# Performance work log

Measured on AMD Instinct MI355X. Metric: run time of the kernel, lower is better.

The kernel has to match this reference:

```python
import jax, jax.numpy as jnp
import numpy as np

B, S, H = 2, 2048, 2048
NH, NKV = 16, 4
HD = H // NH            # 128
GROUPS = NH // NKV      # 4
ROTARY_BASE = 10000.0
NEG = -1e9


def setup_inputs() -> dict:
    key = jax.random.key(0)
    ks = jax.random.split(key, 6)
    x = jax.random.normal(ks[0], (B, S, H), dtype=jnp.float32)
    # additive causal mask [B,1,S,S]
    causal = jnp.where(jnp.tril(jnp.ones((S, S), dtype=bool)), 0.0, NEG).astype(jnp.float32)
    attention_mask = jnp.broadcast_to(causal[None, None], (B, 1, S, S))
    position_ids = jnp.broadcast_to(jnp.arange(S, dtype=jnp.int32)[None], (B, S))
    sc = 0.02
    Wq = jax.random.normal(ks[1], (H, NH * HD), dtype=jnp.float32) * sc
    Wk = jax.random.normal(ks[2], (H, NKV * HD), dtype=jnp.float32) * sc
    Wv = jax.random.normal(ks[3], (H, NKV * HD), dtype=jnp.float32) * sc
    Wo = jax.random.normal(ks[4], (H, H), dtype=jnp.float32) * sc
    return {"x": x, "attention_mask": attention_mask, "position_ids": position_ids,
            "Wq": Wq, "Wk": Wk, "Wv": Wv, "Wo": Wo}


def _rotate_half(t):
    t1, t2 = t[..., : HD // 2], t[..., HD // 2:]
    return jnp.concatenate((-t2, t1), axis=-1)


def _rope_sin_cos(position_ids, dtype):
    inv_freq = 1.0 / (ROTARY_BASE ** (jnp.arange(0, HD, 2, dtype=jnp.float32) / HD))  # [HD/2]
    freqs = position_ids.astype(jnp.float32)[..., None] * inv_freq[None, None, :]      # [B,S,HD/2]
    emb = jnp.concatenate((freqs, freqs), axis=-1)                                     # [B,S,HD]
    return jnp.sin(emb).astype(dtype), jnp.cos(emb).astype(dtype)


def reference(x, attention_mask, position_ids, Wq, Wk, Wv, Wo):
    # QKV projections (no bias)
    q = (x @ Wq).reshape(B, S, NH, HD).transpose(0, 2, 1, 3)     # [B,NH,S,HD]
    k = (x @ Wk).reshape(B, S, NKV, HD).transpose(0, 2, 1, 3)    # [B,NKV,S,HD]
    v = (x @ Wv).reshape(B, S, NKV, HD).transpose(0, 2, 1, 3)
    sin, cos = _rope_sin_cos(position_ids, x.dtype)
    sin, cos = sin[:, None], cos[:, None]                         # unsqueeze head dim
    q = q * cos + _rotate_half(q) * sin
    k = k * cos + _rotate_half(k) * sin
    # GQA: repeat kv heads
    k = jnp.repeat(k, GROUPS, axis=1)                             # [B,NH,S,HD]
    v = jnp.repeat(v, GROUPS, axis=1)
    scores = jnp.einsum('bhqd,bhkd->bhqk', q, k) / jnp.sqrt(jnp.asarray(HD, x.dtype))
    scores = scores + attention_mask                              # additive causal mask
    attn = jax.nn.softmax(scores.astype(jnp.float32), axis=-1).astype(x.dtype)
    # dropout p=0.0 -> no-op
    out = jnp.einsum('bhqk,bhkd->bhqd', attn, v)                  # [B,NH,S,HD]
    out = out.transpose(0, 2, 1, 3).reshape(B, S, H)
    return out @ Wo
```

## Files before the change

kernel.cpp:

```cpp
#include <hip/hip_runtime.h>
#include <hip/hip_bf16.h>
#include <stdint.h>
#include <math.h>

#define B_ 2
#define S_ 2048
#define H_ 2048
#define NH_ 16
#define NKV_ 4
#define HD_ 128

typedef __bf16 bf16;
typedef __bf16 bf16x8 __attribute__((ext_vector_type(8)));
typedef __bf16 bf16x4 __attribute__((ext_vector_type(4)));
typedef float f32x4 __attribute__((ext_vector_type(4)));

__device__ __forceinline__ void async_copy16(const void* g, void* l) {
  __builtin_amdgcn_global_load_lds(
      (const __attribute__((address_space(1))) void*)(uintptr_t)g,
      (__attribute__((address_space(3))) void*)(uintptr_t)l,
      16, 0, 0);
}

__device__ __forceinline__ f32x4 mfma16(bf16x8 a, bf16x8 b, f32x4 c) {
  return __builtin_amdgcn_mfma_f32_16x16x32_bf16(a, b, c, 0, 0, 0);
}


__global__ void f32_to_bf16_k(const float* __restrict__ in, bf16* __restrict__ o, int n) {
  int i = (blockIdx.x * 256 + threadIdx.x) * 4;
  if (i >= n) return;
  float4 v = *(const float4*)(in + i);
  bf16x4 r;
  r[0] = (bf16)v.x; r[1] = (bf16)v.y; r[2] = (bf16)v.z; r[3] = (bf16)v.w;
  *(bf16x4*)(o + i) = r;
}

__global__ void transpose_to_bf16_k(const float* __restrict__ W, bf16* __restrict__ Wt,
                                    int K, int N) {
  __shared__ float tile[32][33];
  int n0 = blockIdx.x * 32, k0 = blockIdx.y * 32;
  int tx = threadIdx.x, ty = threadIdx.y;
#pragma unroll
  for (int j = 0; j < 32; j += 8)
    tile[ty + j][tx] = W[(size_t)(k0 + ty + j) * N + n0 + tx];
  __syncthreads();
#pragma unroll
  for (int j = 0; j < 32; j += 8)
    Wt[(size_t)(n0 + ty + j) * K + k0 + tx] = (bf16)tile[tx][ty + j];
}

__global__ void rope_table_k(float2* __restrict__ tab) {
  int i = blockIdx.x * 256 + threadIdx.x;
  int p = i >> 6, d = i & 63;
  float invf = expf(-((float)(2 * d) / 128.0f) * 9.210340371976184f);
  float fr = (float)p * invf;
  float sv, cv;
  sincosf(fr, &sv, &cv);
  tab[i] = make_float2(cv, sv);
}

__global__ void rope_apply_k(bf16* __restrict__ t, const int* __restrict__ pos_ids,
                             const float2* __restrict__ tab, int hshift, int hmask,
                             float scale) {
  int i = blockIdx.x * 256 + threadIdx.x;
  int d = i & 63;
  int tmp = i >> 6;
  int h = tmp & hmask;
  int row = tmp >> hshift;
  int pos = pos_ids[row];
  float2 cs = tab[pos * 64 + d];
  size_t base = (((size_t)row << hshift) + h) * HD_;
  float a = (float)t[base + d];
  float b = (float)t[base + d + 64];
  t[base + d]      = (bf16)((a * cs.x - b * cs.y) * scale);
  t[base + d + 64] = (bf16)((b * cs.x + a * cs.y) * scale);
}


template <int MODE>
__global__ __launch_bounds__(512) void gemm8_k(const bf16* __restrict__ A,
                                               const bf16* __restrict__ Bt,
                                               void* __restrict__ C0,
                                               void* __restrict__ C1,
                                               void* __restrict__ C2,
                                               int M, int N, int K) {
  extern __shared__ __align__(16) char smem[];
  const int tid = threadIdx.x;
  const int lane = tid & 63;
  const int w = tid >> 6;
  const int wm = w >> 2;
  const int wn = w & 3;
  const int g16 = lane >> 4, c16 = lane & 15;
  const int row0 = blockIdx.y * 128;
  const int col0 = blockIdx.x * 256;
  const int srow = tid >> 3;
  const int sslot = tid & 7;
  const int ldsw = w * 1024;

  auto stageA = [&](int s, int kt, int r) {
    int row = r * 64 + srow;
    int ss = sslot ^ (row & 7);
    async_copy16(A + (size_t)(row0 + row) * K + (kt << 6) + ss * 8,
                 smem + s * 49152 + r * 8192 + ldsw);
  };
  auto stageB = [&](int s, int kt, int r) {
    int row = r * 64 + srow;
    int ss = sslot ^ (row & 7);
    async_copy16(Bt + (size_t)(col0 + row) * K + (kt << 6) + ss * 8,
                 smem + s * 49152 + 16384 + r * 8192 + ldsw);
  };

  int offA[2][4], offB[2][4];
#pragma unroll
  for (int ks = 0; ks < 2; ++ks) {
#pragma unroll
    for (int i = 0; i < 4; ++i) {
      int ra = wm * 64 + i * 16 + c16;
      offA[ks][i] = ra * 128 + (((ks * 4 + g16) ^ (ra & 7)) << 4);
      int rb = wn * 64 + i * 16 + c16;
      offB[ks][i] = rb * 128 + (((ks * 4 + g16) ^ (rb & 7)) << 4);
    }
  }

  const f32x4 fz = {0.f, 0.f, 0.f, 0.f};
  f32x4 acc[4][4];
#pragma unroll
  for (int i = 0; i < 4; ++i)
#pragma unroll
    for (int j = 0; j < 4; ++j) acc[i][j] = fz;

  const int nkt = K >> 6;
#pragma unroll
  for (int r = 0; r < 2; ++r) stageA(0, 0, r);
#pragma unroll
  for (int r = 0; r < 4; ++r) stageB(0, 0, r);
#pragma unroll
  for (int r = 0; r < 2; ++r) stageA(1, 1, r);
#pragma unroll
  for (int r = 0; r < 4; ++r) stageB(1, 1, r);
  asm volatile("s_waitcnt vmcnt(6)" ::: "memory");
  __builtin_amdgcn_s_barrier();

  int ct = 0, pt = 2;
  for (int t = 0; t < nkt; ++t) {
    const char* Ab = smem + ct * 49152;
    const char* Bb = Ab + 16384;
    const bool pf = (t + 2 < nkt);
    const int kpf = t + 2;
    bf16x8 af[4], bfr[4];

#pragma unroll
    for (int i = 0; i < 4; ++i) af[i] = *(const bf16x8*)(Ab + offA[0][i]);
#pragma unroll
    for (int j = 0; j < 4; ++j) bfr[j] = *(const bf16x8*)(Bb + offB[0][j]);
    if (pf) { stageA(pt, kpf, 0); stageA(pt, kpf, 1); stageB(pt, kpf, 0); }
    __builtin_amdgcn_s_barrier();
    asm volatile("s_waitcnt lgkmcnt(0)" ::: "memory");
    __builtin_amdgcn_sched_barrier(0);
    __builtin_amdgcn_s_setprio(1);
#pragma unroll
    for (int i = 0; i < 4; ++i)
#pragma unroll
      for (int j = 0; j < 4; ++j) acc[i][j] = mfma16(af[i], bfr[j], acc[i][j]);
    __builtin_amdgcn_s_setprio(0);
    __builtin_amdgcn_sched_barrier(0);
    __builtin_amdgcn_s_barrier();

#pragma unroll
    for (int i = 0; i < 4; ++i) af[i] = *(const bf16x8*)(Ab + offA[1][i]);
#pragma unroll
    for (int j = 0; j < 4; ++j) bfr[j] = *(const bf16x8*)(Bb + offB[1][j]);
    if (pf) { stageB(pt, kpf, 1); stageB(pt, kpf, 2); stageB(pt, kpf, 3); }
    if (pf) asm volatile("s_waitcnt vmcnt(6)" ::: "memory");
    else    asm volatile("s_waitcnt vmcnt(0)" ::: "memory");
    __builtin_amdgcn_s_barrier();
    asm volatile("s_waitcnt lgkmcnt(0)" ::: "memory");
    __builtin_amdgcn_sched_barrier(0);
    __builtin_amdgcn_s_setprio(1);
#pragma unroll
    for (int i = 0; i < 4; ++i)
#pragma unroll
      for (int j = 0; j < 4; ++j) acc[i][j] = mfma16(af[i], bfr[j], acc[i][j]);
    __builtin_amdgcn_s_setprio(0);
    __builtin_amdgcn_sched_barrier(0);
    __builtin_amdgcn_s_barrier();

    ct = (ct == 2) ? 0 : ct + 1;
    pt = (pt == 2) ? 0 : pt + 1;
  }

#pragma unroll
  for (int i = 0; i < 4; ++i) {
    int gr0 = row0 + wm * 64 + i * 16 + g16 * 4;
#pragma unroll
    for (int j = 0; j < 4; ++j) {
      int gc = col0 + wn * 64 + j * 16 + c16;
      if constexpr (MODE == 2) {
        if (col0 < 2048) {
#pragma unroll
          for (int r = 0; r < 4; ++r)
            ((bf16*)C0)[(size_t)(gr0 + r) * 2048 + gc] = (bf16)acc[i][j][r];
        } else if (col0 < 2560) {
#pragma unroll
          for (int r = 0; r < 4; ++r)
            ((bf16*)C1)[(size_t)(gr0 + r) * 512 + (gc - 2048)] = (bf16)acc[i][j][r];
        } else {
          int dv = gc - 2560;
          int hkv = dv >> 7, d = dv & 127;
          size_t va = (((size_t)(gr0 >> 11) * NKV_ + hkv) * HD_ + d) * S_ + (gr0 & 2047);
          bf16x4 pk;
#pragma unroll
          for (int r = 0; r < 4; ++r) pk[r] = (bf16)acc[i][j][r];
          *(bf16x4*)((bf16*)C2 + va) = pk;
        }
      } else {
#pragma unroll
        for (int r = 0; r < 4; ++r) {
          if constexpr (MODE == 1)
            ((float*)C0)[(size_t)(gr0 + r) * N + gc] = acc[i][j][r];
          else
            ((bf16*)C0)[(size_t)(gr0 + r) * N + gc] = (bf16)acc[i][j][r];
        }
      }
    }
  }
}


template <bool OUT_F32, bool VT_Z1>
__global__ __launch_bounds__(256) void gemm_bt_k(const bf16* __restrict__ A,
                                                 const bf16* __restrict__ Bt0,
                                                 const bf16* __restrict__ Bt1,
                                                 void* __restrict__ C0, void* __restrict__ C1,
                                                 int M, int N, int K) {
  const bf16* __restrict__ Bt = (blockIdx.z == 0) ? Bt0 : Bt1;
  void* C = (blockIdx.z == 0) ? C0 : C1;
  __shared__ __align__(16) bf16 As[128 * 64];
  __shared__ __align__(16) bf16 Bs[128 * 64];
  const int tid = threadIdx.x;
  const int lane = tid & 63;
  const int w = tid >> 6;
  const int wm = w >> 1, wn = w & 1;
  const int g16 = lane >> 4, c16 = lane & 15;
  const int row0 = blockIdx.y * 128;
  const int col0 = blockIdx.x * 128;
  const int sr = lane >> 3;
  const int st = lane & 7;
  const int ss = st ^ sr;

  const f32x4 fz = {0.f, 0.f, 0.f, 0.f};
  f32x4 acc[4][4];
#pragma unroll
  for (int i = 0; i < 4; ++i)
#pragma unroll
    for (int j = 0; j < 4; ++j) acc[i][j] = fz;

  const int nkt = K >> 6;
  for (int kt = 0; kt < nkt; ++kt) {
    const int k0 = kt << 6;
    __syncthreads();
#pragma unroll
    for (int c = 0; c < 4; ++c) {
      int rbase = w * 32 + c * 8;
      async_copy16(A + (size_t)(row0 + rbase + sr) * K + k0 + ss * 8,
                   (char*)As + rbase * 128);
      async_copy16(Bt + (size_t)(col0 + rbase + sr) * K + k0 + ss * 8,
                   (char*)Bs + rbase * 128);
    }
    __syncthreads();
#pragma unroll
    for (int ks = 0; ks < 2; ++ks) {
      bf16x8 af[4], bfr[4];
#pragma unroll
      for (int t = 0; t < 4; ++t) {
        int ra = wm * 64 + t * 16 + c16;
        af[t] = *(const bf16x8*)((const char*)As + ra * 128 + (((ks * 4 + g16) ^ (ra & 7)) << 4));
        int rb = wn * 64 + t * 16 + c16;
        bfr[t] = *(const bf16x8*)((const char*)Bs + rb * 128 + (((ks * 4 + g16) ^ (rb & 7)) << 4));
      }
#pragma unroll
      for (int i = 0; i < 4; ++i)
#pragma unroll
        for (int j = 0; j < 4; ++j) acc[i][j] = mfma16(af[i], bfr[j], acc[i][j]);
    }
  }

  const bool vt = VT_Z1 && (blockIdx.z == 1);
#pragma unroll
  for (int i = 0; i < 4; ++i) {
    int gr0 = row0 + wm * 64 + i * 16 + g16 * 4;
#pragma unroll
    for (int j = 0; j < 4; ++j) {
      int gc = col0 + wn * 64 + j * 16 + c16;
      if (vt) {
        size_t va = ((size_t)((gr0 >> 11) * NKV_ + (gc >> 7)) * HD_ + (gc & 127)) * S_ + (gr0 & 2047);
        bf16x4 pk;
#pragma unroll
        for (int r = 0; r < 4; ++r) pk[r] = (bf16)acc[i][j][r];
        *(bf16x4*)((bf16*)C + va) = pk;
      } else {
#pragma unroll
        for (int r = 0; r < 4; ++r) {
          if constexpr (OUT_F32)
            ((float*)C)[(size_t)(gr0 + r) * N + gc] = acc[i][j][r];
          else
            ((bf16*)C)[(size_t)(gr0 + r) * N + gc] = (bf16)acc[i][j][r];
        }
      }
    }
  }
}


__global__ __launch_bounds__(256, 2) void attn_fwd_k(const bf16* __restrict__ Qg,
                                                     const bf16* __restrict__ Kg,
                                                     const bf16* __restrict__ VTg,
                                                     bf16* __restrict__ Og) {
  __shared__ __align__(16) bf16 Ks[2][64 * 128];
  __shared__ __align__(16) bf16 Vt[2][128 * 64];

  const int tid = threadIdx.x;
  const int lane = tid & 63;
  const int w = tid >> 6;
  const int g16 = lane >> 4;
  const int c16 = lane & 15;

  int bid = blockIdx.x;
  int rr_ = bid >> 5, bh = bid & 31;
  int qb = (rr_ < 8) ? (15 - rr_) : (rr_ - 8);
  const int b = bh >> 4;
  const int h = bh & 15;
  const int hkv = h >> 2;
  const int q0 = qb * 128;
  const int qw = q0 + w * 32;

  bf16x8 qf[2][4];
#pragma unroll
  for (int nq = 0; nq < 2; ++nq)
#pragma unroll
    for (int ksq = 0; ksq < 4; ++ksq)
      qf[nq][ksq] = *(const bf16x8*)(Qg + ((size_t)(b * S_ + qw + nq * 16 + c16) * NH_ + h) * HD_ + (ksq * 4 + g16) * 8);

  float m_run[2] = {-1e30f, -1e30f};
  float l_run[2] = {0.f, 0.f};
  const f32x4 fz = {0.f, 0.f, 0.f, 0.f};
  f32x4 acc[2][8];
#pragma unroll
  for (int nq = 0; nq < 2; ++nq)
#pragma unroll
    for (int dt = 0; dt < 8; ++dt) acc[nq][dt] = fz;

  const size_t kbase = ((size_t)b * S_ * NKV_ + hkv) * HD_;
  const size_t vbase = ((size_t)(b * NKV_ + hkv)) * HD_ * S_;

  auto stage = [&](int buf, int kv0) {
#pragma unroll
    for (int rd = 0; rd < 4; ++rd) {
      int Lb = rd * 256 + w * 64;
      int row = (Lb + lane) >> 4;
      int ssl = (lane & 15) ^ (row & 7);
      async_copy16(Kg + kbase + (size_t)(kv0 + row) * (NKV_ * HD_) + ssl * 8,
                   (char*)&Ks[buf][0] + Lb * 16);
    }
#pragma unroll
    for (int rd = 0; rd < 4; ++rd) {
      int Lb = rd * 256 + w * 64;
      int row = (Lb + lane) >> 3;
      int ssl = (lane & 7) ^ (row & 7);
      async_copy16(VTg + vbase + (size_t)row * S_ + kv0 + ssl * 8,
                   (char*)&Vt[buf][0] + Lb * 16);
    }
  };

  const int ntiles = 2 * qb + 2;
  stage(0, 0);
  int cur = 0;

  for (int t = 0; t < ntiles; ++t) {
    __syncthreads();
    if (t + 1 < ntiles) stage(cur ^ 1, (t + 1) * 64);
    const int kv0 = t * 64;

    if (kv0 <= qw + 31) {
      const bf16* KsC = &Ks[cur][0];
      const bf16* VtC = &Vt[cur][0];

      f32x4 sc[2][4];
#pragma unroll
      for (int nq = 0; nq < 2; ++nq)
#pragma unroll
        for (int mt = 0; mt < 4; ++mt) sc[nq][mt] = fz;

      __builtin_amdgcn_s_setprio(1);
#pragma unroll
      for (int ksq = 0; ksq < 4; ++ksq) {
        bf16x8 kf[4];
#pragma unroll
        for (int mt = 0; mt < 4; ++mt) {
          int gp = c16 >> 2, rp = c16 & 3;
          int blk = 8 * (mt >> 1) + 2 * gp + ((mt & 1) ^ (gp & 1));
          int row = blk * 4 + rp;
          kf[mt] = *(const bf16x8*)((const char*)KsC + row * 256 + (((ksq * 4 + g16) ^ (row & 7)) << 4));
        }
#pragma unroll
        for (int nq = 0; nq < 2; ++nq)
#pragma unroll
          for (int mt = 0; mt < 4; ++mt)
            sc[nq][mt] = mfma16(kf[mt], qf[nq][ksq], sc[nq][mt]);
      }
      __builtin_amdgcn_s_setprio(0);

      if (kv0 + 63 > qw) {
#pragma unroll
        for (int nq = 0; nq < 2; ++nq) {
          int qa = qw + nq * 16 + c16;
#pragma unroll
          for (int mt = 0; mt < 4; ++mt) {
            int blk = 8 * (mt >> 1) + 2 * g16 + ((mt & 1) ^ (g16 & 1));
#pragma unroll
            for (int r = 0; r < 4; ++r) {
              int ka = kv0 + blk * 4 + r;
              if (ka > qa) sc[nq][mt][r] = -1e30f;
            }
          }
        }
      }

      float mx[2];
#pragma unroll
      for (int nq = 0; nq < 2; ++nq) {
        float v = sc[nq][0][0];
#pragma unroll
        for (int mt = 0; mt < 4; ++mt)
#pragma unroll
          for (int r = 0; r < 4; ++r) v = fmaxf(v, sc[nq][mt][r]);
        v = fmaxf(v, __shfl_xor(v, 16));
        v = fmaxf(v, __shfl_xor(v, 32));
        mx[nq] = v;
      }
      if (__any((mx[0] > m_run[0] + 8.f) || (mx[1] > m_run[1] + 8.f))) {
#pragma unroll
        for (int nq = 0; nq < 2; ++nq) {
          float mn = fmaxf(m_run[nq], mx[nq]);
          float corr = exp2f(m_run[nq] - mn);
          m_run[nq] = mn;
          l_run[nq] *= corr;
#pragma unroll
          for (int dt = 0; dt < 8; ++dt) acc[nq][dt] *= corr;
        }
      }
#pragma unroll
      for (int nq = 0; nq < 2; ++nq) {
        float sum = 0.f;
#pragma unroll
        for (int mt = 0; mt < 4; ++mt)
#pragma unroll
          for (int r = 0; r < 4; ++r) {
            float p = exp2f(sc[nq][mt][r] - m_run[nq]);
            sc[nq][mt][r] = p;
            sum += p;
          }
        sum += __shfl_xor(sum, 16);
        sum += __shfl_xor(sum, 32);
        l_run[nq] += sum;
      }

      bf16x8 pa[2][2];
#pragma unroll
      for (int nq = 0; nq < 2; ++nq)
#pragma unroll
        for (int ks = 0; ks < 2; ++ks) {
          f32x4 sA = (g16 & 1) ? sc[nq][2 * ks + 1] : sc[nq][2 * ks];
          f32x4 sB = (g16 & 1) ? sc[nq][2 * ks] : sc[nq][2 * ks + 1];
          bf16x8 tf;
          tf[0] = (bf16)sA[0]; tf[1] = (bf16)sA[1]; tf[2] = (bf16)sA[2]; tf[3] = (bf16)sA[3];
          tf[4] = (bf16)sB[0]; tf[5] = (bf16)sB[1]; tf[6] = (bf16)sB[2]; tf[7] = (bf16)sB[3];
          pa[nq][ks] = tf;
        }

      __builtin_amdgcn_s_setprio(1);
#pragma unroll
      for (int ks = 0; ks < 2; ++ks)
#pragma unroll
        for (int dt = 0; dt < 8; ++dt) {
          int rv = dt * 16 + c16;
          bf16x8 vf = *(const bf16x8*)((const char*)VtC + rv * 128 + (((ks * 4 + g16) ^ (rv & 7)) << 4));
          acc[0][dt] = mfma16(vf, pa[0][ks], acc[0][dt]);
          acc[1][dt] = mfma16(vf, pa[1][ks], acc[1][dt]);
        }
      __builtin_amdgcn_s_setprio(0);
    }
    cur ^= 1;
  }

#pragma unroll
  for (int nq = 0; nq < 2; ++nq) {
    float inv = 1.0f / l_run[nq];
    size_t base = ((size_t)(b * S_ + qw + nq * 16 + c16) * NH_ + h) * HD_ + g16 * 4;
#pragma unroll
    for (int dt = 0; dt < 8; ++dt) {
      bf16x4 ov;
#pragma unroll
      for (int r = 0; r < 4; ++r) ov[r] = (bf16)(acc[nq][dt][r] * inv);
      *(bf16x4*)(Og + base + dt * 16) = ov;
    }
  }
}


extern "C" void kernel_launch(void* const* d_in, const int* in_sizes, int n_in,
                              void* d_out, int out_size, void* d_ws, size_t ws_size,
                              hipStream_t stream) {
  const float* x  = (const float*)d_in[0];
  const int* pos  = (const int*)d_in[2];
  const float* Wq = (const float*)d_in[3];
  const float* Wk = (const float*)d_in[4];
  const float* Wv = (const float*)d_in[5];
  const float* Wo = (const float*)d_in[6];

  char* ws = (char*)d_ws;
  size_t off = 0;
  auto alloc = [&](size_t bytes) -> char* {
    char* p = ws + off;
    off += (bytes + 255) & ~(size_t)255;
    return p;
  };
  const size_t rows = (size_t)B_ * S_;
  bf16* xb    = (bf16*)alloc(rows * H_ * 2);
  bf16* bq    = (bf16*)alloc(rows * (NH_ * HD_) * 2);
  bf16* batt  = (bf16*)alloc(rows * (NH_ * HD_) * 2);
  bf16* WqkvT = (bf16*)alloc((size_t)3072 * H_ * 2);
  bf16* WoT   = (bf16*)alloc((size_t)H_ * H_ * 2);
  bf16* bk    = (bf16*)alloc(rows * (NKV_ * HD_) * 2);
  bf16* VT    = (bf16*)alloc(rows * (NKV_ * HD_) * 2);
  float2* tab = (float2*)alloc((size_t)S_ * 64 * sizeof(float2));

  bf16* WqT = WqkvT;
  bf16* WkT = WqkvT + (size_t)2048 * H_;
  bf16* WvT = WqkvT + (size_t)2560 * H_;

  auto* fqkv = gemm8_k<2>;
  auto* fo   = gemm8_k<1>;
  const int dynlds = 3 * 49152;
  bool big =
      (hipFuncSetAttribute((const void*)fqkv, hipFuncAttributeMaxDynamicSharedMemorySize, dynlds) == hipSuccess) &&
      (hipFuncSetAttribute((const void*)fo, hipFuncAttributeMaxDynamicSharedMemorySize, dynlds) == hipSuccess);

  f32_to_bf16_k<<<(rows * H_) / (256 * 4), 256, 0, stream>>>(x, xb, rows * H_);
  transpose_to_bf16_k<<<dim3(H_ / 32, H_ / 32), dim3(32, 8), 0, stream>>>(Wq, WqT, H_, NH_ * HD_);
  transpose_to_bf16_k<<<dim3((NKV_ * HD_) / 32, H_ / 32), dim3(32, 8), 0, stream>>>(Wk, WkT, H_, NKV_ * HD_);
  transpose_to_bf16_k<<<dim3((NKV_ * HD_) / 32, H_ / 32), dim3(32, 8), 0, stream>>>(Wv, WvT, H_, NKV_ * HD_);
  transpose_to_bf16_k<<<dim3(H_ / 32, H_ / 32), dim3(32, 8), 0, stream>>>(Wo, WoT, H_, H_);
  rope_table_k<<<(S_ * 64) / 256, 256, 0, stream>>>(tab);

  if (big) {
    gemm8_k<2><<<dim3(12, 32), 512, dynlds, stream>>>(xb, WqkvT, bq, bk, VT, 4096, 3072, 2048);
  } else {
    gemm_bt_k<false, false><<<dim3(16, 32, 1), 256, 0, stream>>>(xb, WqT, WqT, bq, bq, 4096, 2048, 2048);
    gemm_bt_k<false, true><<<dim3(4, 32, 2), 256, 0, stream>>>(xb, WkT, WvT, bk, VT, 4096, 512, 2048);
  }

  rope_apply_k<<<(4096 * NH_ * 64) / 256, 256, 0, stream>>>(bq, pos, tab, 4, 15, 0.12753102f);
  rope_apply_k<<<(4096 * NKV_ * 64) / 256, 256, 0, stream>>>(bk, pos, tab, 2, 3, 1.0f);

  attn_fwd_k<<<dim3(512), 256, 0, stream>>>(bq, bk, VT, batt);

  if (big)
    gemm8_k<1><<<dim3(8, 32), 512, dynlds, stream>>>(batt, WoT, d_out, nullptr, nullptr, 4096, 2048, 2048);
  else
    gemm_bt_k<true, false><<<dim3(16, 32, 1), 256, 0, stream>>>(batt, WoT, WoT, d_out, d_out, 4096, 2048, 2048);
}
```

Before: 219.8 us.

## Use 256x256-tile double-buffered GEMM kernel for fused QKV projection

Adds a new GEMM kernel with a 256x256 output tile per 512-thread block and a double-buffered 128KB LDS pipeline. Loads for the next K-tile are split across the four compute phases, and it is used for the fused QKV projection. The larger tile raises arithmetic intensity and cuts global/L2 traffic for A and B. The cost is more accumulator registers (128 floats per thread), lower occupancy, and fewer blocks (192 versus 384), which could underfill the 256 CUs.

```diff
diff --git a/kernel.cpp b/kernel.cpp
--- a/kernel.cpp
+++ b/kernel.cpp
@@ -75,6 +75,160 @@
   float b = (float)t[base + d + 64];
   t[base + d]      = (bf16)((a * cs.x - b * cs.y) * scale);
   t[base + d + 64] = (bf16)((b * cs.x + a * cs.y) * scale);
+}
+
+
+template <int MODE>
+__global__ __launch_bounds__(512) void gemm256_k(const bf16* __restrict__ A,
+                                                 const bf16* __restrict__ Bt,
+                                                 void* __restrict__ C0,
+                                                 void* __restrict__ C1,
+                                                 void* __restrict__ C2,
+                                                 int M, int N, int K) {
+  extern __shared__ __align__(16) char smem[];
+  const int tid = threadIdx.x;
+  const int lane = tid & 63;
+  const int w = tid >> 6;
+  const int wm = w >> 2;
+  const int wn = w & 3;
+  const int g16 = lane >> 4, c16 = lane & 15;
+  const int row0 = blockIdx.y * 256;
+  const int col0 = blockIdx.x * 256;
+  const int srow = tid >> 3;
+  const int sslot = tid & 7;
+  const int ldsw = w * 1024;
+
+  auto stage = [&](int buf, int kt, int r) {
+    int row = (r & 3) * 64 + srow;
+    int ss = sslot ^ (row & 7);
+    const bf16* src = (r < 4) ? (A + (size_t)(row0 + row) * K)
+                              : (Bt + (size_t)(col0 + row) * K);
+    async_copy16(src + (kt << 6) + ss * 8,
+                 smem + buf * 65536 + (r >> 2) * 32768 + (r & 3) * 8192 + ldsw);
+  };
+
+  int offA[2][8], offB[2][4];
+#pragma unroll
+  for (int ks = 0; ks < 2; ++ks) {
+#pragma unroll
+    for (int i = 0; i < 8; ++i) {
+      int ra = wm * 128 + i * 16 + c16;
+      offA[ks][i] = ra * 128 + (((ks * 4 + g16) ^ (ra & 7)) << 4);
+    }
+#pragma unroll
+    for (int j = 0; j < 4; ++j) {
+      int rb = wn * 64 + j * 16 + c16;
+      offB[ks][j] = 32768 + rb * 128 + (((ks * 4 + g16) ^ (rb & 7)) << 4);
+    }
+  }
+
+  const f32x4 fz = {0.f, 0.f, 0.f, 0.f};
+  f32x4 acc[8][4];
+#pragma unroll
+  for (int i = 0; i < 8; ++i)
+#pragma unroll
+    for (int j = 0; j < 4; ++j) acc[i][j] = fz;
+
+  const int nkt = K >> 6;
+#pragma unroll
+  for (int r = 0; r < 8; ++r) stage(0, 0, r);
+  asm volatile("s_waitcnt vmcnt(0)" ::: "memory");
+  __builtin_amdgcn_s_barrier();
+
+  for (int t = 0; t < nkt; ++t) {
+    const char* Ab = smem + (t & 1) * 65536;
+    const bool pf = (t + 1 < nkt);
+    const int nb = (t + 1) & 1;
+    bf16x8 bfr[2][4];
+
+    {
+      bf16x8 af[2][2];
+#pragma unroll
+      for (int ks = 0; ks < 2; ++ks) {
+#pragma unroll
+        for (int j = 0; j < 4; ++j) bfr[ks][j] = *(const bf16x8*)(Ab + offB[ks][j]);
+        af[ks][0] = *(const bf16x8*)(Ab + offA[ks][0]);
+        af[ks][1] = *(const bf16x8*)(Ab + offA[ks][1]);
+      }
+      if (pf) { stage(nb, t + 1, 0); stage(nb, t + 1, 1); stage(nb, t + 1, 2); stage(nb, t + 1, 3); }
+      __builtin_amdgcn_s_barrier();
+      asm volatile("s_waitcnt lgkmcnt(0)" ::: "memory");
+      __builtin_amdgcn_sched_barrier(0);
+      __builtin_amdgcn_s_setprio(1);
+#pragma unroll
+      for (int ks = 0; ks < 2; ++ks)
+#pragma unroll
+        for (int m = 0; m < 2; ++m)
+#pragma unroll
+          for (int j = 0; j < 4; ++j)
+            acc[m][j] = mfma16(af[ks][m], bfr[ks][j], acc[m][j]);
+      __builtin_amdgcn_s_setprio(0);
+      __builtin_amdgcn_sched_barrier(0);
+      __builtin_amdgcn_s_barrier();
+    }
+
+#pragma unroll
+    for (int q = 1; q < 4; ++q) {
+      bf16x8 af[2][2];
+#pragma unroll
+      for (int ks = 0; ks < 2; ++ks) {
+        af[ks][0] = *(const bf16x8*)(Ab + offA[ks][q * 2]);
+        af[ks][1] = *(const bf16x8*)(Ab + offA[ks][q * 2 + 1]);
+      }
+      if (q == 1 && pf) { stage(nb, t + 1, 4); stage(nb, t + 1, 5); stage(nb, t + 1, 6); stage(nb, t + 1, 7); }
+      __builtin_amdgcn_s_barrier();
+      asm volatile("s_waitcnt lgkmcnt(0)" ::: "memory");
+      __builtin_amdgcn_sched_barrier(0);
+      __builtin_amdgcn_s_setprio(1);
+#pragma unroll
+      for (int ks = 0; ks < 2; ++ks)
+#pragma unroll
+        for (int m = 0; m < 2; ++m)
+#pragma unroll
+          for (int j = 0; j < 4; ++j)
+            acc[q * 2 + m][j] = mfma16(af[ks][m], bfr[ks][j], acc[q * 2 + m][j]);
+      __builtin_amdgcn_s_setprio(0);
+      __builtin_amdgcn_sched_barrier(0);
+      if (q == 3 && pf) asm volatile("s_waitcnt vmcnt(0)" ::: "memory");
+      __builtin_amdgcn_s_barrier();
+    }
+  }
+
+#pragma unroll
+  for (int i = 0; i < 8; ++i) {
+    int gr0 = row0 + wm * 128 + i * 16 + g16 * 4;
+#pragma unroll
+    for (int j = 0; j < 4; ++j) {
+      int gc = col0 + wn * 64 + j * 16 + c16;
+      if constexpr (MODE == 2) {
+        if (col0 < 2048) {
+#pragma unroll
+          for (int r = 0; r < 4; ++r)
+            ((bf16*)C0)[(size_t)(gr0 + r) * 2048 + gc] = (bf16)acc[i][j][r];
+        } else if (col0 < 2560) {
+#pragma unroll
+          for (int r = 0; r < 4; ++r)
+            ((bf16*)C1)[(size_t)(gr0 + r) * 512 + (gc - 2048)] = (bf16)acc[i][j][r];
+        } else {
+          int dv = gc - 2560;
+          int hkv = dv >> 7, d = dv & 127;
+          size_t va = (((size_t)(gr0 >> 11) * NKV_ + hkv) * HD_ + d) * S_ + (gr0 & 2047);
+          bf16x4 pk;
+#pragma unroll
+          for (int r = 0; r < 4; ++r) pk[r] = (bf16)acc[i][j][r];
+          *(bf16x4*)((bf16*)C2 + va) = pk;
+        }
+      } else {
+#pragma unroll
+        for (int r = 0; r < 4; ++r) {
+          if constexpr (MODE == 1)
+            ((float*)C0)[(size_t)(gr0 + r) * N + gc] = acc[i][j][r];
+          else
+            ((bf16*)C0)[(size_t)(gr0 + r) * N + gc] = (bf16)acc[i][j][r];
+        }
+      }
+    }
+  }
 }
 
 
@@ -196,32 +350,12 @@
 #pragma unroll
     for (int j = 0; j < 4; ++j) {
       int gc = col0 + wn * 64 + j * 16 + c16;
-      if constexpr (MODE == 2) {
-        if (col0 < 2048) {
-#pragma unroll
-          for (int r = 0; r < 4; ++r)
-            ((bf16*)C0)[(size_t)(gr0 + r) * 2048 + gc] = (bf16)acc[i][j][r];
-        } else if (col0 < 2560) {
-#pragma unroll
-          for (int r = 0; r < 4; ++r)
-            ((bf16*)C1)[(size_t)(gr0 + r) * 512 + (gc - 2048)] = (bf16)acc[i][j][r];
-        } else {
-          int dv = gc - 2560;
-          int hkv = dv >> 7, d = dv & 127;
-          size_t va = (((size_t)(gr0 >> 11) * NKV_ + hkv) * HD_ + d) * S_ + (gr0 & 2047);
-          bf16x4 pk;
-#pragma unroll
-          for (int r = 0; r < 4; ++r) pk[r] = (bf16)acc[i][j][r];
-          *(bf16x4*)((bf16*)C2 + va) = pk;
-        }
-      } else {
-#pragma unroll
-        for (int r = 0; r < 4; ++r) {
-          if constexpr (MODE == 1)
-            ((float*)C0)[(size_t)(gr0 + r) * N + gc] = acc[i][j][r];
-          else
-            ((bf16*)C0)[(size_t)(gr0 + r) * N + gc] = (bf16)acc[i][j][r];
-        }
+#pragma unroll
+      for (int r = 0; r < 4; ++r) {
+        if constexpr (MODE == 1)
+          ((float*)C0)[(size_t)(gr0 + r) * N + gc] = acc[i][j][r];
+        else
+          ((bf16*)C0)[(size_t)(gr0 + r) * N + gc] = (bf16)acc[i][j][r];
       }
     }
   }
@@ -540,12 +674,13 @@
   bf16* WkT = WqkvT + (size_t)2048 * H_;
   bf16* WvT = WqkvT + (size_t)2560 * H_;
 
-  auto* fqkv = gemm8_k<2>;
+  auto* fqkv = gemm256_k<2>;
   auto* fo   = gemm8_k<1>;
-  const int dynlds = 3 * 49152;
+  const int lds256 = 2 * 65536;
+  const int lds8   = 3 * 49152;
   bool big =
-      (hipFuncSetAttribute((const void*)fqkv, hipFuncAttributeMaxDynamicSharedMemorySize, dynlds) == hipSuccess) &&
-      (hipFuncSetAttribute((const void*)fo, hipFuncAttributeMaxDynamicSharedMemorySize, dynlds) == hipSuccess);
+      (hipFuncSetAttribute((const void*)fqkv, hipFuncAttributeMaxDynamicSharedMemorySize, lds256) == hipSuccess) &&
+      (hipFuncSetAttribute((const void*)fo, hipFuncAttributeMaxDynamicSharedMemorySize, lds8) == hipSuccess);
 
   f32_to_bf16_k<<<(rows * H_) / (256 * 4), 256, 0, stream>>>(x, xb, rows * H_);
   transpose_to_bf16_k<<<dim3(H_ / 32, H_ / 32), dim3(32, 8), 0, stream>>>(Wq, WqT, H_, NH_ * HD_);
@@ -555,7 +690,7 @@
   rope_table_k<<<(S_ * 64) / 256, 256, 0, stream>>>(tab);
 
   if (big) {
-    gemm8_k<2><<<dim3(12, 32), 512, dynlds, stream>>>(xb, WqkvT, bq, bk, VT, 4096, 3072, 2048);
+    gemm256_k<2><<<dim3(12, 16), 512, lds256, stream>>>(xb, WqkvT, bq, bk, VT, 4096, 3072, 2048);
   } else {
     gemm_bt_k<false, false><<<dim3(16, 32, 1), 256, 0, stream>>>(xb, WqT, WqT, bq, bq, 4096, 2048, 2048);
     gemm_bt_k<false, true><<<dim3(4, 32, 2), 256, 0, stream>>>(xb, WkT, WvT, bk, VT, 4096, 512, 2048);
@@ -567,7 +702,7 @@
   attn_fwd_k<<<dim3(512), 256, 0, stream>>>(bq, bk, VT, batt);
 
   if (big)
-    gemm8_k<1><<<dim3(8, 32), 512, dynlds, stream>>>(batt, WoT, d_out, nullptr, nullptr, 4096, 2048, 2048);
+    gemm8_k<1><<<dim3(8, 32), 512, lds8, stream>>>(batt, WoT, d_out, nullptr, nullptr, 4096, 2048, 2048);
   else
     gemm_bt_k<true, false><<<dim3(16, 32, 1), 256, 0, stream>>>(batt, WoT, WoT, d_out, d_out, 4096, 2048, 2048);
 }
```

After: 212.5 us. 1.03x faster.
